# Kernel tuning notes

Measured on AMD Instinct MI355X. Metric: run time of the kernel, lower is better.

## Reference

```python
import jax, jax.numpy as jnp
import numpy as np
from itertools import combinations

B, F, E, V = 4096, 39, 40, 1000000
BN_EPS = 1e-3  # tf.layers.batch_normalization default epsilon


def setup_inputs() -> dict:
    key = jax.random.key(0)
    k_in, k_w, k_v, k_e = jax.random.split(key, 4)
    inputs = jax.random.randint(k_in, (B, F), 0, V, dtype=jnp.int64)
    # generate_pairs(range(F)): cols = first elements, rows = second elements
    pairs = np.array(list(combinations(range(F), 2)), dtype=np.int64)  # [741, 2]
    cols = jnp.asarray(pairs[:, 0])
    rows = jnp.asarray(pairs[:, 1])
    w = jax.random.normal(k_w, (V,), dtype=jnp.float32) * 0.01
    v = jax.random.normal(k_v, (V, E), dtype=jnp.float32) * (1.0 / np.sqrt(E))
    b = jnp.zeros((), dtype=jnp.float32)
    # edge weights init ~ uniform(weight_base - 1e-3, weight_base + 1e-3)
    edge_weights = jax.random.uniform(k_e, (pairs.shape[0],), dtype=jnp.float32,
                                      minval=0.599, maxval=0.601)
    return {"inputs": inputs, "rows": rows, "cols": cols,
            "w": w, "v": v, "b": b, "edge_weights": edge_weights}


def reference(inputs, rows, cols, w, v, b, edge_weights):
    # Embedding lookups
    xw = w[inputs]                      # [B, F]  first-order weights
    xv = v[inputs]                      # [B, F, E] second-order embeddings
    l = jnp.sum(xw, axis=1)             # [B] linear term

    # Pairwise FM interactions: gather field pairs, multiply, reduce over embed
    left = xv[:, rows]                  # [B, P, E]
    right = xv[:, cols]                 # [B, P, E]
    level_2 = jnp.sum(left * right, axis=-1)  # [B, P]

    # BatchNorm (training mode, scale=False, center=False): batch stats per pair
    mean = jnp.mean(level_2, axis=0)
    var = jnp.var(level_2, axis=0)      # biased variance, as in TF BN
    level_2 = (level_2 - mean) * jax.lax.rsqrt(var + BN_EPS)

    # Edge-weight (architecture) mask
    level_2 = level_2 * edge_weights[None, :]

    fm_out = jnp.sum(level_2, axis=-1)  # [B]
    logits = l + fm_out + b             # [B]
    return logits
```

## Files before the change

kernel.cpp:

```cpp
#include <hip/hip_runtime.h>

#define NF 39
#define NE 40
#define NB 4096
#define NSLOT 1536
#define K1_BLOCKS 512
#define SPW 2
#define SPB 8
#define K2A_COLB 12
#define K2A_ROWG 8

typedef __attribute__((ext_vector_type(8))) short short8;
typedef __attribute__((ext_vector_type(4))) float floatx4;

__device__ __forceinline__ unsigned int f2bf(float f) {
    unsigned int b = __float_as_uint(f);
    b += 0x7FFFu + ((b >> 16) & 1u);
    return b >> 16;
}

__device__ __forceinline__ short8 pack8(float4 a, float4 b) {
    union { unsigned int u[4]; short8 s; } o;
    o.u[0] = f2bf(a.x) | (f2bf(a.y) << 16);
    o.u[1] = f2bf(a.z) | (f2bf(a.w) << 16);
    o.u[2] = f2bf(b.x) | (f2bf(b.y) << 16);
    o.u[3] = f2bf(b.z) | (f2bf(b.w) << 16);
    return o.s;
}

__device__ __forceinline__ void load_frags(
    const int* __restrict__ ip, const float* __restrict__ v,
    int rbase, int ehalf, short8 F0[3], short8 F1[3])
{
    const float4 zero4 = {0.f, 0.f, 0.f, 0.f};
#pragma unroll
    for (int I = 0; I < 3; ++I) {
        const int r = rbase + 16 * I;
        const bool vr = (r < NF);
        const int id = vr ? ip[r] : 0;
        const float* vrow = v + (size_t)id * NE;
        const float4 a  = vr ? *reinterpret_cast<const float4*>(vrow + ehalf * 8)     : zero4;
        const float4 bq = vr ? *reinterpret_cast<const float4*>(vrow + ehalf * 8 + 4) : zero4;
        F0[I] = pack8(a, bq);
        const bool v1 = vr && (ehalf == 0);
        const float4 c_ = v1 ? *reinterpret_cast<const float4*>(vrow + 32) : zero4;
        const float4 d_ = v1 ? *reinterpret_cast<const float4*>(vrow + 36) : zero4;
        F1[I] = pack8(c_, d_);
    }
}

__device__ __forceinline__ void gram_mfma(const short8 F0[3], const short8 F1[3], floatx4 acc[6])
{
    acc[0] = __builtin_amdgcn_mfma_f32_16x16x32_bf16(F0[0], F0[0], acc[0], 0, 0, 0);
    acc[1] = __builtin_amdgcn_mfma_f32_16x16x32_bf16(F0[0], F0[1], acc[1], 0, 0, 0);
    acc[2] = __builtin_amdgcn_mfma_f32_16x16x32_bf16(F0[0], F0[2], acc[2], 0, 0, 0);
    acc[3] = __builtin_amdgcn_mfma_f32_16x16x32_bf16(F0[1], F0[1], acc[3], 0, 0, 0);
    acc[4] = __builtin_amdgcn_mfma_f32_16x16x32_bf16(F0[1], F0[2], acc[4], 0, 0, 0);
    acc[5] = __builtin_amdgcn_mfma_f32_16x16x32_bf16(F0[2], F0[2], acc[5], 0, 0, 0);
    acc[0] = __builtin_amdgcn_mfma_f32_16x16x32_bf16(F1[0], F1[0], acc[0], 0, 0, 0);
    acc[1] = __builtin_amdgcn_mfma_f32_16x16x32_bf16(F1[0], F1[1], acc[1], 0, 0, 0);
    acc[2] = __builtin_amdgcn_mfma_f32_16x16x32_bf16(F1[0], F1[2], acc[2], 0, 0, 0);
    acc[3] = __builtin_amdgcn_mfma_f32_16x16x32_bf16(F1[1], F1[1], acc[3], 0, 0, 0);
    acc[4] = __builtin_amdgcn_mfma_f32_16x16x32_bf16(F1[1], F1[2], acc[4], 0, 0, 0);
    acc[5] = __builtin_amdgcn_mfma_f32_16x16x32_bf16(F1[2], F1[2], acc[5], 0, 0, 0);
}

__global__ __launch_bounds__(256) void fm_k1(
    const int* __restrict__ inputs, const float* __restrict__ v,
    float* __restrict__ partial)
{
    __shared__ float red[4 * 2 * NSLOT];
    const int t = threadIdx.x, wid = t >> 6, lane = t & 63;
    const int rbase = lane & 15, ehalf = lane >> 4;
    const int b0 = blockIdx.x * SPB;

    floatx4 sum[6] = {}, sq[6] = {};
#pragma unroll
    for (int s = 0; s < SPW; ++s) {
        const int* ip = inputs + (size_t)(b0 + wid * SPW + s) * NF;
        short8 F0[3], F1[3];
        load_frags(ip, v, rbase, ehalf, F0, F1);
        floatx4 acc[6] = {};
        gram_mfma(F0, F1, acc);
#pragma unroll
        for (int tl = 0; tl < 6; ++tl) {
            sum[tl] += acc[tl];
            sq[tl]  += acc[tl] * acc[tl];
        }
    }

    float* rw = &red[wid * 2 * NSLOT];
#pragma unroll
    for (int tl = 0; tl < 6; ++tl) {
        *reinterpret_cast<floatx4*>(rw + tl * 256 + lane * 4)         = sum[tl];
        *reinterpret_cast<floatx4*>(rw + NSLOT + tl * 256 + lane * 4) = sq[tl];
    }
    __syncthreads();
    float* po = partial + (size_t)blockIdx.x * (2 * NSLOT);
    for (int j = t; j < 2 * NSLOT; j += 256)
        po[j] = red[j] + red[2 * NSLOT + j] + red[4 * NSLOT + j] + red[6 * NSLOT + j];
}

__global__ __launch_bounds__(256) void fm_k2a(
    const float* __restrict__ partial, float* __restrict__ partial2)
{
    const int col = blockIdx.x * 256 + threadIdx.x;
    const int r0  = blockIdx.y * 64;
    float s = 0.0f;
#pragma unroll 8
    for (int r = 0; r < 64; ++r)
        s += partial[(size_t)(r0 + r) * (2 * NSLOT) + col];
    partial2[(size_t)blockIdx.y * (2 * NSLOT) + col] = s;
}

__global__ __launch_bounds__(256) void fm_k2b(
    const float* __restrict__ partial2, const float* __restrict__ ew,
    float* __restrict__ meanArr, float* __restrict__ scaleArr)
{
    const int slot = blockIdx.x * 256 + threadIdx.x;
    float s1 = 0.f, s2 = 0.f;
#pragma unroll
    for (int ry = 0; ry < K2A_ROWG; ++ry) {
        s1 += partial2[(size_t)ry * (2 * NSLOT) + slot];
        s2 += partial2[(size_t)ry * (2 * NSLOT) + NSLOT + slot];
    }
    const float m   = s1 * (1.0f / NB);
    const float var = s2 * (1.0f / NB) - m * m;
    const int tile = slot >> 8;
    const int l    = (slot & 255) >> 2;
    const int q    = slot & 3;
    const int TI[6] = {0, 0, 0, 1, 1, 2};
    const int TJ[6] = {0, 1, 2, 1, 2, 2};
    const int gi = 16 * TI[tile] + ((l >> 4) << 2) + q;
    const int gj = 16 * TJ[tile] + (l & 15);
    float scl = 0.0f;
    if (gi < gj && gj < NF) {
        const int p = 38 * gi - (gi * (gi - 1)) / 2 + (gj - gi - 1);
        scl = ew[p] * rsqrtf(var + 1.0e-3f);
    }
    meanArr[slot]  = m;
    scaleArr[slot] = scl;
}

__global__ __launch_bounds__(256) void fm_k3(
    const int* __restrict__ inputs, const float* __restrict__ w,
    const float* __restrict__ v, const float* __restrict__ meanArr,
    const float* __restrict__ scaleArr, const float* __restrict__ bias,
    float* __restrict__ out)
{
    const int t = threadIdx.x, wid = t >> 6, lane = t & 63;
    const int rbase = lane & 15, ehalf = lane >> 4;
    const int b0 = blockIdx.x * SPB;

    floatx4 mf[6], sf[6];
#pragma unroll
    for (int tl = 0; tl < 6; ++tl) {
        mf[tl] = *reinterpret_cast<const floatx4*>(meanArr  + tl * 256 + lane * 4);
        sf[tl] = *reinterpret_cast<const floatx4*>(scaleArr + tl * 256 + lane * 4);
    }
    const float bs = bias[0];

#pragma unroll
    for (int s = 0; s < SPW; ++s) {
        const int smp = b0 + wid * SPW + s;
        const int* ip = inputs + (size_t)smp * NF;
        short8 F0[3], F1[3];
        load_frags(ip, v, rbase, ehalf, F0, F1);
        floatx4 acc[6] = {};
        gram_mfma(F0, F1, acc);
        float tot = (lane < NF) ? w[ip[lane]] : 0.0f;
#pragma unroll
        for (int tl = 0; tl < 6; ++tl)
#pragma unroll
            for (int q = 0; q < 4; ++q)
                tot += (acc[tl][q] - mf[tl][q]) * sf[tl][q];
#pragma unroll
        for (int o = 32; o > 0; o >>= 1) tot += __shfl_down(tot, o, 64);
        if (lane == 0) out[smp] = tot + bs;
    }
}

extern "C" void kernel_launch(void* const* d_in, const int* in_sizes, int n_in,
                              void* d_out, int out_size, void* d_ws, size_t ws_size,
                              hipStream_t stream)
{
    const int*   inputs = (const int*)  d_in[0];
    const float* w      = (const float*)d_in[3];
    const float* v      = (const float*)d_in[4];
    const float* bias   = (const float*)d_in[5];
    const float* ew     = (const float*)d_in[6];
    float*       out    = (float*)      d_out;

    float* partial  = (float*)d_ws;
    float* partial2 = partial + (size_t)K1_BLOCKS * 2 * NSLOT;
    float* meanA    = partial2 + (size_t)K2A_ROWG * 2 * NSLOT;
    float* scaleA   = meanA + NSLOT;

    fm_k1 <<<K1_BLOCKS, 256, 0, stream>>>(inputs, v, partial);
    fm_k2a<<<dim3(K2A_COLB, K2A_ROWG), 256, 0, stream>>>(partial, partial2);
    fm_k2b<<<NSLOT / 256, 256, 0, stream>>>(partial2, ew, meanA, scaleA);
    fm_k3 <<<NB / SPB, 256, 0, stream>>>(inputs, w, v, meanA, scaleA, bias, out);
}
```

Before: 34.16 us.

## Cache bf16 fragments in workspace and merge stat-reduction kernels

The first pass now writes the packed bf16 MFMA fragments and the per-sample linear sums to workspace. The final pass reloads these contiguous fragments instead of doing a second random gather from the large embedding table. The two-stage reduction of batch statistics is folded into a single kernel of 48 blocks, which removes one launch. The cost is extra workspace writes, roughly 7.8 MB of fragments, and the stats reduction now runs on fewer blocks.

```diff
diff --git a/kernel.cpp b/kernel.cpp
--- a/kernel.cpp
+++ b/kernel.cpp
@@ -4,11 +4,11 @@
 #define NE 40
 #define NB 4096
 #define NSLOT 1536
-#define K1_BLOCKS 512
+#define NBLK 512
 #define SPW 2
 #define SPB 8
-#define K2A_COLB 12
-#define K2A_ROWG 8
+#define K2_BLOCKS 48
+#define EPS 1.0e-3f
 
 typedef __attribute__((ext_vector_type(8))) short short8;
 typedef __attribute__((ext_vector_type(4))) float floatx4;
@@ -66,7 +66,9 @@
 }
 
 __global__ __launch_bounds__(256) void fm_k1(
-    const int* __restrict__ inputs, const float* __restrict__ v,
+    const int* __restrict__ inputs, const float* __restrict__ w,
+    const float* __restrict__ v, short8* __restrict__ wf0,
+    short8* __restrict__ wf1, float* __restrict__ lsum,
     float* __restrict__ partial)
 {
     __shared__ float red[4 * 2 * NSLOT];
@@ -75,100 +77,116 @@
     const int b0 = blockIdx.x * SPB;
 
     floatx4 sum[6] = {}, sq[6] = {};
-#pragma unroll
-    for (int s = 0; s < SPW; ++s) {
-        const int* ip = inputs + (size_t)(b0 + wid * SPW + s) * NF;
-        short8 F0[3], F1[3];
-        load_frags(ip, v, rbase, ehalf, F0, F1);
-        floatx4 acc[6] = {};
-        gram_mfma(F0, F1, acc);
-#pragma unroll
-        for (int tl = 0; tl < 6; ++tl) {
-            sum[tl] += acc[tl];
-            sq[tl]  += acc[tl] * acc[tl];
-        }
-    }
-
-    float* rw = &red[wid * 2 * NSLOT];
-#pragma unroll
-    for (int tl = 0; tl < 6; ++tl) {
-        *reinterpret_cast<floatx4*>(rw + tl * 256 + lane * 4)         = sum[tl];
-        *reinterpret_cast<floatx4*>(rw + NSLOT + tl * 256 + lane * 4) = sq[tl];
-    }
-    __syncthreads();
-    float* po = partial + (size_t)blockIdx.x * (2 * NSLOT);
-    for (int j = t; j < 2 * NSLOT; j += 256)
-        po[j] = red[j] + red[2 * NSLOT + j] + red[4 * NSLOT + j] + red[6 * NSLOT + j];
-}
-
-__global__ __launch_bounds__(256) void fm_k2a(
-    const float* __restrict__ partial, float* __restrict__ partial2)
-{
-    const int col = blockIdx.x * 256 + threadIdx.x;
-    const int r0  = blockIdx.y * 64;
-    float s = 0.0f;
-#pragma unroll 8
-    for (int r = 0; r < 64; ++r)
-        s += partial[(size_t)(r0 + r) * (2 * NSLOT) + col];
-    partial2[(size_t)blockIdx.y * (2 * NSLOT) + col] = s;
-}
-
-__global__ __launch_bounds__(256) void fm_k2b(
-    const float* __restrict__ partial2, const float* __restrict__ ew,
-    float* __restrict__ meanArr, float* __restrict__ scaleArr)
-{
-    const int slot = blockIdx.x * 256 + threadIdx.x;
-    float s1 = 0.f, s2 = 0.f;
-#pragma unroll
-    for (int ry = 0; ry < K2A_ROWG; ++ry) {
-        s1 += partial2[(size_t)ry * (2 * NSLOT) + slot];
-        s2 += partial2[(size_t)ry * (2 * NSLOT) + NSLOT + slot];
-    }
-    const float m   = s1 * (1.0f / NB);
-    const float var = s2 * (1.0f / NB) - m * m;
-    const int tile = slot >> 8;
-    const int l    = (slot & 255) >> 2;
-    const int q    = slot & 3;
-    const int TI[6] = {0, 0, 0, 1, 1, 2};
-    const int TJ[6] = {0, 1, 2, 1, 2, 2};
-    const int gi = 16 * TI[tile] + ((l >> 4) << 2) + q;
-    const int gj = 16 * TJ[tile] + (l & 15);
-    float scl = 0.0f;
-    if (gi < gj && gj < NF) {
-        const int p = 38 * gi - (gi * (gi - 1)) / 2 + (gj - gi - 1);
-        scl = ew[p] * rsqrtf(var + 1.0e-3f);
-    }
-    meanArr[slot]  = m;
-    scaleArr[slot] = scl;
-}
-
-__global__ __launch_bounds__(256) void fm_k3(
-    const int* __restrict__ inputs, const float* __restrict__ w,
-    const float* __restrict__ v, const float* __restrict__ meanArr,
-    const float* __restrict__ scaleArr, const float* __restrict__ bias,
-    float* __restrict__ out)
-{
-    const int t = threadIdx.x, wid = t >> 6, lane = t & 63;
-    const int rbase = lane & 15, ehalf = lane >> 4;
-    const int b0 = blockIdx.x * SPB;
-
-    floatx4 mf[6], sf[6];
-#pragma unroll
-    for (int tl = 0; tl < 6; ++tl) {
-        mf[tl] = *reinterpret_cast<const floatx4*>(meanArr  + tl * 256 + lane * 4);
-        sf[tl] = *reinterpret_cast<const floatx4*>(scaleArr + tl * 256 + lane * 4);
-    }
-    const float bs = bias[0];
-
 #pragma unroll
     for (int s = 0; s < SPW; ++s) {
         const int smp = b0 + wid * SPW + s;
         const int* ip = inputs + (size_t)smp * NF;
         short8 F0[3], F1[3];
         load_frags(ip, v, rbase, ehalf, F0, F1);
+#pragma unroll
+        for (int I = 0; I < 3; ++I) {
+            wf0[((size_t)smp * 3 + I) * 64 + lane] = F0[I];
+            if (ehalf == 0) wf1[((size_t)smp * 3 + I) * 16 + rbase] = F1[I];
+        }
+        float wv = (lane < NF) ? w[ip[lane]] : 0.0f;
+#pragma unroll
+        for (int o = 32; o > 0; o >>= 1) wv += __shfl_down(wv, o, 64);
+        if (lane == 0) lsum[smp] = wv;
+
         floatx4 acc[6] = {};
         gram_mfma(F0, F1, acc);
-        float tot = (lane < NF) ? w[ip[lane]] : 0.0f;
+#pragma unroll
+        for (int tl = 0; tl < 6; ++tl) {
+            sum[tl] += acc[tl];
+            sq[tl]  += acc[tl] * acc[tl];
+        }
+    }
+
+    float* rw = &red[wid * 2 * NSLOT];
+#pragma unroll
+    for (int tl = 0; tl < 6; ++tl) {
+        *reinterpret_cast<floatx4*>(rw + tl * 256 + lane * 4)         = sum[tl];
+        *reinterpret_cast<floatx4*>(rw + NSLOT + tl * 256 + lane * 4) = sq[tl];
+    }
+    __syncthreads();
+    float* po = partial + (size_t)blockIdx.x * (2 * NSLOT);
+    for (int j = t; j < 2 * NSLOT; j += 256)
+        po[j] = red[j] + red[2 * NSLOT + j] + red[4 * NSLOT + j] + red[6 * NSLOT + j];
+}
+
+__global__ __launch_bounds__(256) void fm_k2(
+    const float* __restrict__ partial, const float* __restrict__ ew,
+    float* __restrict__ meanArr, float* __restrict__ scaleArr)
+{
+    const int t = threadIdx.x;
+    const int slotL = t & 31, rg = t >> 5;
+    const int slot0 = blockIdx.x * 32;
+    float s1 = 0.f, s2 = 0.f;
+#pragma unroll 8
+    for (int r = 0; r < 64; ++r) {
+        const float* row = partial + (size_t)(rg * 64 + r) * (2 * NSLOT);
+        s1 += row[slot0 + slotL];
+        s2 += row[NSLOT + slot0 + slotL];
+    }
+    __shared__ float r1[8][32], r2[8][32];
+    r1[rg][slotL] = s1;
+    r2[rg][slotL] = s2;
+    __syncthreads();
+    if (t < 32) {
+        float a = 0.f, b = 0.f;
+#pragma unroll
+        for (int g = 0; g < 8; ++g) { a += r1[g][t]; b += r2[g][t]; }
+        const int slot = slot0 + t;
+        const float m   = a * (1.0f / NB);
+        const float var = b * (1.0f / NB) - m * m;
+        const int tile = slot >> 8;
+        const int l    = (slot & 255) >> 2;
+        const int q    = slot & 3;
+        const int TI[6] = {0, 0, 0, 1, 1, 2};
+        const int TJ[6] = {0, 1, 2, 1, 2, 2};
+        const int gi = 16 * TI[tile] + ((l >> 4) << 2) + q;
+        const int gj = 16 * TJ[tile] + (l & 15);
+        float scl = 0.0f;
+        if (gi < gj && gj < NF) {
+            const int p = 38 * gi - (gi * (gi - 1)) / 2 + (gj - gi - 1);
+            scl = ew[p] * rsqrtf(var + EPS);
+        }
+        meanArr[slot]  = m;
+        scaleArr[slot] = scl;
+    }
+}
+
+__global__ __launch_bounds__(256) void fm_k3(
+    const short8* __restrict__ wf0, const short8* __restrict__ wf1,
+    const float* __restrict__ lsum, const float* __restrict__ meanArr,
+    const float* __restrict__ scaleArr, const float* __restrict__ bias,
+    float* __restrict__ out)
+{
+    const int t = threadIdx.x, wid = t >> 6, lane = t & 63;
+    const int rbase = lane & 15, ehalf = lane >> 4;
+    const int b0 = blockIdx.x * SPB;
+
+    floatx4 mf[6], sf[6];
+#pragma unroll
+    for (int tl = 0; tl < 6; ++tl) {
+        mf[tl] = *reinterpret_cast<const floatx4*>(meanArr  + tl * 256 + lane * 4);
+        sf[tl] = *reinterpret_cast<const floatx4*>(scaleArr + tl * 256 + lane * 4);
+    }
+    const float bs = bias[0];
+    const short8 z8 = {0, 0, 0, 0, 0, 0, 0, 0};
+
+#pragma unroll
+    for (int s = 0; s < SPW; ++s) {
+        const int smp = b0 + wid * SPW + s;
+        short8 F0[3], F1[3];
+#pragma unroll
+        for (int I = 0; I < 3; ++I) {
+            F0[I] = wf0[((size_t)smp * 3 + I) * 64 + lane];
+            F1[I] = (ehalf == 0) ? wf1[((size_t)smp * 3 + I) * 16 + rbase] : z8;
+        }
+        floatx4 acc[6] = {};
+        gram_mfma(F0, F1, acc);
+        float tot = (lane == 0) ? lsum[smp] : 0.0f;
 #pragma unroll
         for (int tl = 0; tl < 6; ++tl)
 #pragma unroll
@@ -191,13 +209,14 @@
     const float* ew     = (const float*)d_in[6];
     float*       out    = (float*)      d_out;
 
-    float* partial  = (float*)d_ws;
-    float* partial2 = partial + (size_t)K1_BLOCKS * 2 * NSLOT;
-    float* meanA    = partial2 + (size_t)K2A_ROWG * 2 * NSLOT;
-    float* scaleA   = meanA + NSLOT;
-
-    fm_k1 <<<K1_BLOCKS, 256, 0, stream>>>(inputs, v, partial);
-    fm_k2a<<<dim3(K2A_COLB, K2A_ROWG), 256, 0, stream>>>(partial, partial2);
-    fm_k2b<<<NSLOT / 256, 256, 0, stream>>>(partial2, ew, meanA, scaleA);
-    fm_k3 <<<NB / SPB, 256, 0, stream>>>(inputs, w, v, meanA, scaleA, bias, out);
-}
+    short8* wf0 = (short8*)d_ws;
+    short8* wf1 = wf0 + (size_t)NB * 3 * 64;
+    float* partial = (float*)(wf1 + (size_t)NB * 3 * 16);
+    float* meanA   = partial + (size_t)NBLK * 2 * NSLOT;
+    float* scaleA  = meanA + NSLOT;
+    float* lsum    = scaleA + NSLOT;
+
+    fm_k1<<<NBLK,      256, 0, stream>>>(inputs, w, v, wf0, wf1, lsum, partial);
+    fm_k2<<<K2_BLOCKS, 256, 0, stream>>>(partial, ew, meanA, scaleA);
+    fm_k3<<<NBLK,      256, 0, stream>>>(wf0, wf1, lsum, meanA, scaleA, bias, out);
+}
```

New measurement: 32.40 us. 5.1% less time.

## Materialize per-sample pair Gram values once instead of recomputing in final pass

Applied to the files above, without the earlier changes.

The first kernel now computes each sample's field-pair dot products once with MFMA and stores the 741 compact pair values per sample to a workspace buffer. It also writes the per-sample linear term. Batch statistics are then reduced from this buffer, and the final kernel reads it back rather than re-gathering embeddings and redoing the MFMA. This removes the second random embedding gather and Gram computation, at the cost of writing and twice re-reading a roughly 12 MB intermediate with scattered scalar stores. Padding slots 741 to 767 are never written, so the final pass multiplies uninitialized values by a zero scale.

```diff
diff --git a/kernel.cpp b/kernel.cpp
--- a/kernel.cpp
+++ b/kernel.cpp
@@ -3,12 +3,13 @@
 #define NF 39
 #define NE 40
 #define NB 4096
-#define NSLOT 1536
-#define K1_BLOCKS 512
-#define SPW 2
-#define SPB 8
-#define K2A_COLB 12
-#define K2A_ROWG 8
+#define NP 741
+#define GST 768
+#define K1_BLOCKS 1024
+#define K2A_BLOCKS 128
+#define K2A_ROWS 32
+#define K3_BLOCKS 512
+#define EPS 1.0e-3f
 
 typedef __attribute__((ext_vector_type(8))) short short8;
 typedef __attribute__((ext_vector_type(4))) float floatx4;
@@ -66,114 +67,116 @@
 }
 
 __global__ __launch_bounds__(256) void fm_k1(
-    const int* __restrict__ inputs, const float* __restrict__ v,
-    float* __restrict__ partial)
-{
-    __shared__ float red[4 * 2 * NSLOT];
+    const int* __restrict__ inputs, const float* __restrict__ w,
+    const float* __restrict__ v, float* __restrict__ Gp,
+    float* __restrict__ lsum)
+{
     const int t = threadIdx.x, wid = t >> 6, lane = t & 63;
     const int rbase = lane & 15, ehalf = lane >> 4;
-    const int b0 = blockIdx.x * SPB;
-
-    floatx4 sum[6] = {}, sq[6] = {};
-#pragma unroll
-    for (int s = 0; s < SPW; ++s) {
-        const int* ip = inputs + (size_t)(b0 + wid * SPW + s) * NF;
-        short8 F0[3], F1[3];
-        load_frags(ip, v, rbase, ehalf, F0, F1);
-        floatx4 acc[6] = {};
-        gram_mfma(F0, F1, acc);
-#pragma unroll
-        for (int tl = 0; tl < 6; ++tl) {
-            sum[tl] += acc[tl];
-            sq[tl]  += acc[tl] * acc[tl];
+    const int smp = blockIdx.x * 4 + wid;
+
+    const int TI[6] = {0, 0, 0, 1, 1, 2};
+    const int TJ[6] = {0, 1, 2, 1, 2, 2};
+    int pv[6][4];
+#pragma unroll
+    for (int tl = 0; tl < 6; ++tl)
+#pragma unroll
+        for (int q = 0; q < 4; ++q) {
+            const int gi = 16 * TI[tl] + 4 * ehalf + q;
+            const int gj = 16 * TJ[tl] + rbase;
+            pv[tl][q] = (gi < gj && gj < NF)
+                      ? (38 * gi - (gi * (gi - 1)) / 2 + (gj - gi - 1)) : -1;
         }
-    }
-
-    float* rw = &red[wid * 2 * NSLOT];
-#pragma unroll
-    for (int tl = 0; tl < 6; ++tl) {
-        *reinterpret_cast<floatx4*>(rw + tl * 256 + lane * 4)         = sum[tl];
-        *reinterpret_cast<floatx4*>(rw + NSLOT + tl * 256 + lane * 4) = sq[tl];
-    }
-    __syncthreads();
-    float* po = partial + (size_t)blockIdx.x * (2 * NSLOT);
-    for (int j = t; j < 2 * NSLOT; j += 256)
-        po[j] = red[j] + red[2 * NSLOT + j] + red[4 * NSLOT + j] + red[6 * NSLOT + j];
+
+    const int* ip = inputs + (size_t)smp * NF;
+    short8 F0[3], F1[3];
+    load_frags(ip, v, rbase, ehalf, F0, F1);
+    floatx4 acc[6] = {};
+    gram_mfma(F0, F1, acc);
+
+    float wv = (lane < NF) ? w[ip[lane]] : 0.0f;
+#pragma unroll
+    for (int o = 32; o > 0; o >>= 1) wv += __shfl_down(wv, o, 64);
+    if (lane == 0) lsum[smp] = wv;
+
+    float* gr = Gp + (size_t)smp * GST;
+#pragma unroll
+    for (int tl = 0; tl < 6; ++tl)
+#pragma unroll
+        for (int q = 0; q < 4; ++q)
+            if (pv[tl][q] >= 0) gr[pv[tl][q]] = acc[tl][q];
 }
 
 __global__ __launch_bounds__(256) void fm_k2a(
-    const float* __restrict__ partial, float* __restrict__ partial2)
-{
-    const int col = blockIdx.x * 256 + threadIdx.x;
-    const int r0  = blockIdx.y * 64;
-    float s = 0.0f;
-#pragma unroll 8
-    for (int r = 0; r < 64; ++r)
-        s += partial[(size_t)(r0 + r) * (2 * NSLOT) + col];
-    partial2[(size_t)blockIdx.y * (2 * NSLOT) + col] = s;
+    const float* __restrict__ Gp, float* __restrict__ partial2)
+{
+    const int t = threadIdx.x;
+    const int r0 = blockIdx.x * K2A_ROWS;
+    float s[3] = {}, q[3] = {};
+    for (int r = 0; r < K2A_ROWS; ++r) {
+        const float* row = Gp + (size_t)(r0 + r) * GST;
+#pragma unroll
+        for (int c = 0; c < 3; ++c) {
+            const float x = row[t + 256 * c];
+            s[c] += x;
+            q[c] = fmaf(x, x, q[c]);
+        }
+    }
+    float* p = partial2 + (size_t)blockIdx.x * 2 * GST;
+#pragma unroll
+    for (int c = 0; c < 3; ++c) {
+        p[t + 256 * c]       = s[c];
+        p[GST + t + 256 * c] = q[c];
+    }
 }
 
 __global__ __launch_bounds__(256) void fm_k2b(
     const float* __restrict__ partial2, const float* __restrict__ ew,
-    float* __restrict__ meanArr, float* __restrict__ scaleArr)
-{
-    const int slot = blockIdx.x * 256 + threadIdx.x;
+    float* __restrict__ meanP, float* __restrict__ scaleP)
+{
+    const int p = blockIdx.x * 256 + threadIdx.x;
+    if (p >= NP) return;
     float s1 = 0.f, s2 = 0.f;
-#pragma unroll
-    for (int ry = 0; ry < K2A_ROWG; ++ry) {
-        s1 += partial2[(size_t)ry * (2 * NSLOT) + slot];
-        s2 += partial2[(size_t)ry * (2 * NSLOT) + NSLOT + slot];
+#pragma unroll 8
+    for (int i = 0; i < K2A_BLOCKS; ++i) {
+        const float* pp = partial2 + (size_t)i * 2 * GST;
+        s1 += pp[p];
+        s2 += pp[GST + p];
     }
     const float m   = s1 * (1.0f / NB);
     const float var = s2 * (1.0f / NB) - m * m;
-    const int tile = slot >> 8;
-    const int l    = (slot & 255) >> 2;
-    const int q    = slot & 3;
-    const int TI[6] = {0, 0, 0, 1, 1, 2};
-    const int TJ[6] = {0, 1, 2, 1, 2, 2};
-    const int gi = 16 * TI[tile] + ((l >> 4) << 2) + q;
-    const int gj = 16 * TJ[tile] + (l & 15);
-    float scl = 0.0f;
-    if (gi < gj && gj < NF) {
-        const int p = 38 * gi - (gi * (gi - 1)) / 2 + (gj - gi - 1);
-        scl = ew[p] * rsqrtf(var + 1.0e-3f);
-    }
-    meanArr[slot]  = m;
-    scaleArr[slot] = scl;
+    meanP[p]  = m;
+    scaleP[p] = ew[p] * rsqrtf(var + EPS);
 }
 
 __global__ __launch_bounds__(256) void fm_k3(
-    const int* __restrict__ inputs, const float* __restrict__ w,
-    const float* __restrict__ v, const float* __restrict__ meanArr,
-    const float* __restrict__ scaleArr, const float* __restrict__ bias,
-    float* __restrict__ out)
+    const float* __restrict__ Gp, const float* __restrict__ lsum,
+    const float* __restrict__ meanP, const float* __restrict__ scaleP,
+    const float* __restrict__ bias, float* __restrict__ out)
 {
     const int t = threadIdx.x, wid = t >> 6, lane = t & 63;
-    const int rbase = lane & 15, ehalf = lane >> 4;
-    const int b0 = blockIdx.x * SPB;
-
-    floatx4 mf[6], sf[6];
-#pragma unroll
-    for (int tl = 0; tl < 6; ++tl) {
-        mf[tl] = *reinterpret_cast<const floatx4*>(meanArr  + tl * 256 + lane * 4);
-        sf[tl] = *reinterpret_cast<const floatx4*>(scaleArr + tl * 256 + lane * 4);
+    const int b0 = blockIdx.x * 8;
+
+    float mv[12], sv[12];
+#pragma unroll
+    for (int k = 0; k < 12; ++k) {
+        const int p = lane + 64 * k;
+        const bool val = (p < NP);
+        mv[k] = val ? meanP[p] : 0.0f;
+        sv[k] = val ? scaleP[p] : 0.0f;
     }
     const float bs = bias[0];
 
 #pragma unroll
-    for (int s = 0; s < SPW; ++s) {
-        const int smp = b0 + wid * SPW + s;
-        const int* ip = inputs + (size_t)smp * NF;
-        short8 F0[3], F1[3];
-        load_frags(ip, v, rbase, ehalf, F0, F1);
-        floatx4 acc[6] = {};
-        gram_mfma(F0, F1, acc);
-        float tot = (lane < NF) ? w[ip[lane]] : 0.0f;
-#pragma unroll
-        for (int tl = 0; tl < 6; ++tl)
-#pragma unroll
-            for (int q = 0; q < 4; ++q)
-                tot += (acc[tl][q] - mf[tl][q]) * sf[tl][q];
+    for (int s = 0; s < 2; ++s) {
+        const int smp = b0 + wid * 2 + s;
+        const float* gr = Gp + (size_t)smp * GST;
+        float tot = (lane == 0) ? lsum[smp] : 0.0f;
+#pragma unroll
+        for (int k = 0; k < 12; ++k) {
+            const float g = gr[lane + 64 * k];
+            tot += (g - mv[k]) * sv[k];
+        }
 #pragma unroll
         for (int o = 32; o > 0; o >>= 1) tot += __shfl_down(tot, o, 64);
         if (lane == 0) out[smp] = tot + bs;
@@ -191,13 +194,14 @@
     const float* ew     = (const float*)d_in[6];
     float*       out    = (float*)      d_out;
 
-    float* partial  = (float*)d_ws;
-    float* partial2 = partial + (size_t)K1_BLOCKS * 2 * NSLOT;
-    float* meanA    = partial2 + (size_t)K2A_ROWG * 2 * NSLOT;
-    float* scaleA   = meanA + NSLOT;
-
-    fm_k1 <<<K1_BLOCKS, 256, 0, stream>>>(inputs, v, partial);
-    fm_k2a<<<dim3(K2A_COLB, K2A_ROWG), 256, 0, stream>>>(partial, partial2);
-    fm_k2b<<<NSLOT / 256, 256, 0, stream>>>(partial2, ew, meanA, scaleA);
-    fm_k3 <<<NB / SPB, 256, 0, stream>>>(inputs, w, v, meanA, scaleA, bias, out);
-}
+    float* Gp       = (float*)d_ws;
+    float* partial2 = Gp + (size_t)NB * GST;
+    float* meanP    = partial2 + (size_t)K2A_BLOCKS * 2 * GST;
+    float* scaleP   = meanP + GST;
+    float* lsum     = scaleP + GST;
+
+    fm_k1 <<<K1_BLOCKS,  256, 0, stream>>>(inputs, w, v, Gp, lsum);
+    fm_k2a<<<K2A_BLOCKS, 256, 0, stream>>>(Gp, partial2);
+    fm_k2b<<<3,          256, 0, stream>>>(partial2, ew, meanP, scaleP);
+    fm_k3 <<<K3_BLOCKS,  256, 0, stream>>>(Gp, lsum, meanP, scaleP, bias, out);
+}
```

Measured after the change: 38.36 us. 12.3% more time.
